# Kernel optimization log

Hardware: AMD Instinct MI355X
Metric: run time of the kernel (lower is better)

Reference implementation:

```python
import jax, jax.numpy as jnp
import numpy as np

B, L, D_MODEL = 1, 1024, 768
H = 12            # num_heads == num_key_value_heads
FDIM = 16         # feature_dim
HEAD_DIM = D_MODEL // H  # 64
EPS = 1e-12
R2 = np.sqrt(2.0)
RD = np.sqrt(float(FDIM))        # sqrt(16) = 4
RRD = np.sqrt(RD)                # sqrt(4) = 2


def setup_inputs() -> dict:
    key = jax.random.key(0)
    ks = jax.random.split(key, 5)
    s = 1.0 / np.sqrt(D_MODEL)
    return {
        "hidden_states": jax.random.normal(ks[0], (B, L, D_MODEL), dtype=jnp.float32),
        "Wq": jax.random.normal(ks[1], (D_MODEL, H * FDIM), dtype=jnp.float32) * s,
        "Wk": jax.random.normal(ks[2], (D_MODEL, H * FDIM), dtype=jnp.float32) * s,
        "Wv": jax.random.normal(ks[3], (D_MODEL, D_MODEL), dtype=jnp.float32) * s,
        "Wo": jax.random.normal(ks[4], (D_MODEL, D_MODEL), dtype=jnp.float32) * s,
    }


def taylor_exp_feature_map(x):
    # x: (b, h, l, FDIM) -> (b, h, l, 1 + FDIM + FDIM^2)
    x2 = (x[..., :, None] * x[..., None, :]).reshape(*x.shape[:-1], FDIM * FDIM) / R2
    ones = jnp.ones((*x.shape[:-1], 1), dtype=x.dtype)
    return jnp.concatenate([ones, x / RRD, x2 / RD], axis=-1)


def reference(hidden_states, Wq, Wk, Wv, Wo):
    b, l, _ = hidden_states.shape
    q = (hidden_states @ Wq).reshape(b, l, H, FDIM).transpose(0, 2, 1, 3)
    k = (hidden_states @ Wk).reshape(b, l, H, FDIM).transpose(0, 2, 1, 3)
    v = (hidden_states @ Wv).reshape(b, l, H, HEAD_DIM).transpose(0, 2, 1, 3)
    q = taylor_exp_feature_map(q)  # (b,h,l,Dexp)
    k = taylor_exp_feature_map(k)  # (b,h,l,Dexp)
    # causal linear attention: y_t = q_t . cumsum_t(k_s v_s^T) / (q_t . cumsum_t(k_s) + eps)
    kv = k[..., :, None] * v[..., None, :]          # (b,h,l,Dexp,hd)
    kv_cum = jnp.cumsum(kv, axis=2)                  # (b,h,l,Dexp,hd)
    num = jnp.einsum('bhln,bhlnd->bhld', q, kv_cum)  # (b,h,l,hd)
    k_cum = jnp.cumsum(k, axis=2)                    # (b,h,l,Dexp)
    den = jnp.einsum('bhln,bhln->bhl', q, k_cum)[..., None] + EPS
    y = num / den                                    # (b,h,l,hd)
    y = y.transpose(0, 2, 1, 3).reshape(b, l, H * HEAD_DIM)
    return y @ Wo
```

## Files before the change

### kernel.cpp

```cpp
#include <hip/hip_runtime.h>

#define C2 0.17677669529663687f

typedef __attribute__((ext_vector_type(8))) short short8;
typedef __attribute__((ext_vector_type(8))) unsigned short ushort8;
typedef __attribute__((ext_vector_type(4))) float f32x4;

__device__ __forceinline__ unsigned short f2bf(float x) {
    union { float f; unsigned u; } v; v.f = x;
    unsigned r = v.u + 0x7fffu + ((v.u >> 16) & 1u);
    return (unsigned short)(r >> 16);
}
__device__ __forceinline__ float bf2f(unsigned short u) {
    union { unsigned u; float f; } v; v.u = ((unsigned)u) << 16;
    return v.f;
}

__device__ __forceinline__ void gemm_inblk_splitk(
    const float* __restrict__ A, const float* __restrict__ W,
    float* __restrict__ out, int row0, int n0, int outcol0, int ldw, int outld)
{
    __shared__ unsigned short Al[2][2][32][40];
    __shared__ unsigned short Bl[2][2][64][40];
    __shared__ float red[32][65];
    const int tid = threadIdx.x;
    const int g = tid >> 8;
    const int t = tid & 255;
    const int lane = t & 63, w4 = t >> 6;
    const int quad = lane >> 4, lr = lane & 15;
    const int k0base = g * 384;

    f32x4 acc[2] = {{0.f,0.f,0.f,0.f},{0.f,0.f,0.f,0.f}};

    float4 ra, rb[2];
    {
        ra = *(const float4*)&A[(size_t)(row0 + (t >> 3)) * 768 + k0base + (t & 7) * 4];
        #pragma unroll
        for (int l = 0; l < 2; ++l) {
            int idy = t + l * 256;
            rb[l] = *(const float4*)&W[(size_t)(k0base + (idy >> 4)) * ldw + n0 + (idy & 15) * 4];
        }
    }
    {
        *(ushort4*)&Al[g][0][t >> 3][(t & 7) * 4] =
            make_ushort4(f2bf(ra.x), f2bf(ra.y), f2bf(ra.z), f2bf(ra.w));
        #pragma unroll
        for (int l = 0; l < 2; ++l) {
            int idy = t + l * 256;
            int kr = idy >> 4, nq = (idy & 15) * 4;
            int col = (((kr >> 3) ^ ((idy & 15) >> 2)) << 3) | (kr & 7);
            Bl[g][0][nq + 0][col] = f2bf(rb[l].x);
            Bl[g][0][nq + 1][col] = f2bf(rb[l].y);
            Bl[g][0][nq + 2][col] = f2bf(rb[l].z);
            Bl[g][0][nq + 3][col] = f2bf(rb[l].w);
        }
    }
    __syncthreads();

    const int ITER = 12;
    #pragma unroll
    for (int i = 0; i < ITER; ++i) {
        const int cur = i & 1, nxt = cur ^ 1;
        float4 na, nb[2];
        if (i + 1 < ITER) {
            int kn = k0base + (i + 1) * 32;
            na = *(const float4*)&A[(size_t)(row0 + (t >> 3)) * 768 + kn + (t & 7) * 4];
            #pragma unroll
            for (int l = 0; l < 2; ++l) {
                int idy = t + l * 256;
                nb[l] = *(const float4*)&W[(size_t)(kn + (idy >> 4)) * ldw + n0 + (idy & 15) * 4];
            }
        }
        short8 af[2], bfr;
        af[0] = *(const short8*)&Al[g][cur][lr][quad << 3];
        af[1] = *(const short8*)&Al[g][cur][16 + lr][quad << 3];
        {
            int csw = quad ^ (w4 & 3);
            bfr = *(const short8*)&Bl[g][cur][w4 * 16 + lr][csw << 3];
        }
        acc[0] = __builtin_amdgcn_mfma_f32_16x16x32_bf16(af[0], bfr, acc[0], 0, 0, 0);
        acc[1] = __builtin_amdgcn_mfma_f32_16x16x32_bf16(af[1], bfr, acc[1], 0, 0, 0);
        if (i + 1 < ITER) {
            *(ushort4*)&Al[g][nxt][t >> 3][(t & 7) * 4] =
                make_ushort4(f2bf(na.x), f2bf(na.y), f2bf(na.z), f2bf(na.w));
            #pragma unroll
            for (int l = 0; l < 2; ++l) {
                int idy = t + l * 256;
                int kr = idy >> 4, nq = (idy & 15) * 4;
                int col = (((kr >> 3) ^ ((idy & 15) >> 2)) << 3) | (kr & 7);
                Bl[g][nxt][nq + 0][col] = f2bf(nb[l].x);
                Bl[g][nxt][nq + 1][col] = f2bf(nb[l].y);
                Bl[g][nxt][nq + 2][col] = f2bf(nb[l].z);
                Bl[g][nxt][nq + 3][col] = f2bf(nb[l].w);
            }
        }
        __syncthreads();
    }
    if (g == 1) {
        #pragma unroll
        for (int mi = 0; mi < 2; ++mi)
            #pragma unroll
            for (int r = 0; r < 4; ++r)
                red[mi * 16 + quad * 4 + r][w4 * 16 + lr] = acc[mi][r];
    }
    __syncthreads();
    if (g == 0) {
        #pragma unroll
        for (int mi = 0; mi < 2; ++mi)
            #pragma unroll
            for (int r = 0; r < 4; ++r) {
                int rr = mi * 16 + quad * 4 + r;
                out[(size_t)(row0 + rr) * outld + outcol0 + w4 * 16 + lr] =
                    acc[mi][r] + red[rr][w4 * 16 + lr];
            }
    }
}

__global__ __launch_bounds__(512) void gemm_qkv_mfma(
    const float* __restrict__ H, const float* __restrict__ Wq,
    const float* __restrict__ Wk, const float* __restrict__ Wv,
    float* __restrict__ out)
{
    const int nt = blockIdx.x, mt = blockIdx.y;
    const float* W; int ldw, n0;
    if (nt < 3)      { W = Wq; ldw = 192; n0 = nt * 64; }
    else if (nt < 6) { W = Wk; ldw = 192; n0 = (nt - 3) * 64; }
    else             { W = Wv; ldw = 768; n0 = (nt - 6) * 64; }
    gemm_inblk_splitk(H, W, out, mt * 32, n0, nt * 64, ldw, 1152);
}

__global__ __launch_bounds__(512) void gemm_wo_mfma(
    const float* __restrict__ Y, const float* __restrict__ Wo, float* __restrict__ out)
{
    const int nt = blockIdx.x, mt = blockIdx.y;
    gemm_inblk_splitk(Y, Wo, out, mt * 32, nt * 64, nt * 64, 768, 768);
}

__global__ __launch_bounds__(256) void chunk_state_k(
    const float* __restrict__ qkv, unsigned short* __restrict__ St, float* __restrict__ z)
{
    const int c = blockIdx.x, h = blockIdx.y;
    __shared__ float Kc[64][17];
    __shared__ unsigned short Pk[320][72];
    __shared__ unsigned short Vt[80][72];
    const int tid = threadIdx.x;
    const int lane = tid & 63, wave = tid >> 6;
    const int quad = lane >> 4, lr = lane & 15;

    {
        int s = tid >> 2, f4 = (tid & 3) * 4;
        float4 kv = *(const float4*)&qkv[(size_t)(c * 64 + s) * 1152 + 192 + h * 16 + f4];
        Kc[s][f4 + 0] = kv.x; Kc[s][f4 + 1] = kv.y; Kc[s][f4 + 2] = kv.z; Kc[s][f4 + 3] = kv.w;
    }
    #pragma unroll
    for (int l = 0; l < 4; ++l) {
        int idx = tid + l * 256;
        int s = idx >> 4, d4 = (idx & 15) * 4;
        float4 vv = *(const float4*)&qkv[(size_t)(c * 64 + s) * 1152 + 384 + h * 64 + d4];
        Vt[d4 + 0][s] = f2bf(vv.x);
        Vt[d4 + 1][s] = f2bf(vv.y);
        Vt[d4 + 2][s] = f2bf(vv.z);
        Vt[d4 + 3][s] = f2bf(vv.w);
    }
    for (int idx = tid; idx < 16 * 72; idx += 256) {
        int rr = 64 + idx / 72, ss = idx % 72;
        Vt[rr][ss] = (rr == 64 && ss < 64) ? (unsigned short)0x3F80 : (unsigned short)0;
    }
    __syncthreads();
    for (int idx = tid; idx < 2880; idx += 256) {
        int n = idx / 9, s8 = (idx % 9) * 8;
        short8 v8;
        #pragma unroll
        for (int tt = 0; tt < 8; ++tt) {
            int s = s8 + tt;
            float ph = 0.f;
            if (s < 64 && n < 273) {
                if (n == 0) ph = 1.f;
                else if (n < 17) ph = Kc[s][n - 1] * 0.5f;
                else { int m = n - 17; ph = Kc[s][m >> 4] * Kc[s][m & 15] * C2; }
            }
            v8[tt] = (short)f2bf(ph);
        }
        *(short8*)&Pk[n][s8] = v8;
    }
    __syncthreads();

    f32x4 acc[5][5];
    #pragma unroll
    for (int a = 0; a < 5; ++a)
        #pragma unroll
        for (int b = 0; b < 5; ++b) acc[a][b] = (f32x4){0.f, 0.f, 0.f, 0.f};
    #pragma unroll
    for (int ks = 0; ks < 2; ++ks) {
        short8 af[5], bfr[5];
        #pragma unroll
        for (int mt = 0; mt < 5; ++mt)
            af[mt] = *(const short8*)&Vt[mt * 16 + lr][ks * 32 + quad * 8];
        #pragma unroll
        for (int nt = 0; nt < 5; ++nt)
            bfr[nt] = *(const short8*)&Pk[(wave * 5 + nt) * 16 + lr][ks * 32 + quad * 8];
        #pragma unroll
        for (int mt = 0; mt < 5; ++mt)
            #pragma unroll
            for (int nt = 0; nt < 5; ++nt)
                acc[mt][nt] = __builtin_amdgcn_mfma_f32_16x16x32_bf16(af[mt], bfr[nt], acc[mt][nt], 0, 0, 0);
    }
    unsigned short* Sbt = St + (size_t)(h * 16 + c) * 18432;
    float* zb = z + (size_t)(h * 16 + c) * 273;
    #pragma unroll
    for (int nt = 0; nt < 5; ++nt) {
        int n = (wave * 5 + nt) * 16 + lr;
        if (n < 273) {
            #pragma unroll
            for (int mt = 0; mt < 4; ++mt)
                #pragma unroll
                for (int r = 0; r < 4; ++r)
                    Sbt[(mt * 16 + quad * 4 + r) * 288 + n] = f2bf(acc[mt][nt][r]);
            if (quad == 0) zb[n] = acc[4][nt][0];
        }
    }
}

__global__ __launch_bounds__(256) void scan_state_k(unsigned short* __restrict__ St, float* __restrict__ z)
{
    const int NS = 12 * 64 * 273;
    int e = blockIdx.x * 256 + threadIdx.x;
    if (e < NS) {
        int hh = e / (64 * 273), rem = e % (64 * 273);
        int d = rem / 273, n = rem % 273;
        unsigned short* p = St + (size_t)hh * 16 * 18432 + d * 288 + n;
        float run = 0.f;
        #pragma unroll
        for (int c = 0; c < 16; ++c) {
            float v = bf2f(p[c * 18432]);
            p[c * 18432] = f2bf(run);
            run += v;
        }
    } else if (e < NS + 12 * 273) {
        int e2 = e - NS, hh = e2 / 273, n = e2 % 273;
        float* p = z + hh * 16 * 273 + n;
        float run = 0.f;
        #pragma unroll
        for (int c = 0; c < 16; ++c) { float v = p[c * 273]; p[c * 273] = run; run += v; }
    }
}

__global__ __launch_bounds__(256) void chunk_out_k(
    const float* __restrict__ qkv, const unsigned short* __restrict__ St, const float* __restrict__ z,
    float* __restrict__ y)
{
    const int c = blockIdx.x, h = blockIdx.y;
    __shared__ float Qc[64][17];
    __shared__ unsigned short Aq[64][40];
    __shared__ unsigned short Kb[64][40];
    __shared__ unsigned short Pq[64][360];
    __shared__ unsigned short Sv[64][360];
    __shared__ float zl[288];
    __shared__ float dpart[6][64];
    const int tid = threadIdx.x;
    const int lane = tid & 63, wave = tid >> 6;
    const int wm = wave & 1, wn = wave >> 1;
    const int quad = lane >> 4, lr = lane & 15;

    {
        int s = tid >> 2, f4 = (tid & 3) * 4;
        const float* base = &qkv[(size_t)(c * 64 + s) * 1152 + h * 16];
        float4 qv = *(const float4*)&base[f4];
        float4 kv = *(const float4*)&base[192 + f4];
        Qc[s][f4 + 0] = qv.x; Qc[s][f4 + 1] = qv.y; Qc[s][f4 + 2] = qv.z; Qc[s][f4 + 3] = qv.w;
        *(ushort4*)&Aq[s][f4] = make_ushort4(f2bf(qv.x), f2bf(qv.y), f2bf(qv.z), f2bf(qv.w));
        *(ushort4*)&Kb[s][f4] = make_ushort4(f2bf(kv.x), f2bf(kv.y), f2bf(kv.z), f2bf(kv.w));
        *(ushort4*)&Aq[s][16 + (tid & 3) * 4] = make_ushort4(0, 0, 0, 0);
        *(ushort4*)&Kb[s][16 + (tid & 3) * 4] = make_ushort4(0, 0, 0, 0);
    }
    #pragma unroll
    for (int l = 0; l < 4; ++l) {
        int idx = tid + l * 256;
        int s = idx >> 4, d4 = (idx & 15) * 4;
        float4 vv = *(const float4*)&qkv[(size_t)(c * 64 + s) * 1152 + 384 + h * 64 + d4];
        Sv[d4 + 0][288 + s] = f2bf(vv.x);
        Sv[d4 + 1][288 + s] = f2bf(vv.y);
        Sv[d4 + 2][288 + s] = f2bf(vv.z);
        Sv[d4 + 3][288 + s] = f2bf(vv.w);
    }
    const unsigned short* Sgt = St + (size_t)(h * 16 + c) * 18432;
    for (int idx = tid; idx < 64 * 34; idx += 256) {
        int d = idx / 34, n8 = (idx % 34) * 8;
        *(ushort8*)&Sv[d][n8] = *(const ushort8*)&Sgt[d * 288 + n8];
    }
    for (int idx = tid; idx < 64; idx += 256) Sv[idx][272] = Sgt[idx * 288 + 272];
    for (int idx = tid; idx < 64 * 15; idx += 256) {
        int d = idx / 15, n = 273 + idx % 15;
        Sv[d][n] = 0;
    }
    const float* zg = z + (size_t)(h * 16 + c) * 273;
    for (int idx = tid; idx < 288; idx += 256) zl[idx] = (idx < 273) ? zg[idx] : 0.f;
    __syncthreads();

    f32x4 accS[2][2] = {{{0.f,0.f,0.f,0.f},{0.f,0.f,0.f,0.f}},
                        {{0.f,0.f,0.f,0.f},{0.f,0.f,0.f,0.f}}};
    {
        short8 af[2], bfr[2];
        #pragma unroll
        for (int mi = 0; mi < 2; ++mi)
            af[mi] = *(const short8*)&Aq[wm * 32 + mi * 16 + lr][quad * 8];
        #pragma unroll
        for (int ni = 0; ni < 2; ++ni)
            bfr[ni] = *(const short8*)&Kb[wn * 32 + ni * 16 + lr][quad * 8];
        #pragma unroll
        for (int mi = 0; mi < 2; ++mi)
            #pragma unroll
            for (int ni = 0; ni < 2; ++ni)
                accS[mi][ni] = __builtin_amdgcn_mfma_f32_16x16x32_bf16(af[mi], bfr[ni], accS[mi][ni], 0, 0, 0);
    }

    {
        int i = lane;
        float qr[16];
        #pragma unroll
        for (int f = 0; f < 16; ++f) qr[f] = Qc[i][f];
        float dp = 0.f;
        int n0 = wave * 72;
        for (int n = n0; n < n0 + 72; ++n) {
            float ph;
            if (n == 0) ph = 1.f;
            else if (n < 17) ph = qr[n - 1] * 0.5f;
            else if (n < 273) { int m = n - 17; ph = qr[m >> 4] * qr[m & 15] * C2; }
            else ph = 0.f;
            Pq[i][n] = f2bf(ph);
            dp += ph * zl[n];
        }
        dpart[wave][i] = dp;
    }

    #pragma unroll
    for (int mi = 0; mi < 2; ++mi) {
        float rs[4] = {0.f, 0.f, 0.f, 0.f};
        #pragma unroll
        for (int ni = 0; ni < 2; ++ni)
            #pragma unroll
            for (int r = 0; r < 4; ++r) {
                int i = wm * 32 + mi * 16 + quad * 4 + r;
                int j = wn * 32 + ni * 16 + lr;
                float u = accS[mi][ni][r];
                float sc = (j <= i) ? (1.f + 0.25f * u + u * u * (1.f / 32.f)) : 0.f;
                rs[r] += sc;
                Pq[i][288 + j] = f2bf(sc);
            }
        #pragma unroll
        for (int r = 0; r < 4; ++r) {
            float v = rs[r];
            v += __shfl_xor(v, 1);
            v += __shfl_xor(v, 2);
            v += __shfl_xor(v, 4);
            v += __shfl_xor(v, 8);
            if (lr == 0) dpart[4 + wn][wm * 32 + mi * 16 + quad * 4 + r] = v;
        }
    }
    __syncthreads();

    f32x4 acc[2][2] = {{{0.f,0.f,0.f,0.f},{0.f,0.f,0.f,0.f}},
                       {{0.f,0.f,0.f,0.f},{0.f,0.f,0.f,0.f}}};
    #pragma unroll
    for (int ks = 0; ks < 11; ++ks) {
        short8 af[2], bfr[2];
        #pragma unroll
        for (int mi = 0; mi < 2; ++mi)
            af[mi] = *(const short8*)&Pq[wm * 32 + mi * 16 + lr][ks * 32 + quad * 8];
        #pragma unroll
        for (int ni = 0; ni < 2; ++ni)
            bfr[ni] = *(const short8*)&Sv[wn * 32 + ni * 16 + lr][ks * 32 + quad * 8];
        #pragma unroll
        for (int mi = 0; mi < 2; ++mi)
            #pragma unroll
            for (int ni = 0; ni < 2; ++ni)
                acc[mi][ni] = __builtin_amdgcn_mfma_f32_16x16x32_bf16(af[mi], bfr[ni], acc[mi][ni], 0, 0, 0);
    }

    #pragma unroll
    for (int mi = 0; mi < 2; ++mi)
        #pragma unroll
        for (int r = 0; r < 4; ++r) {
            int i = wm * 32 + mi * 16 + quad * 4 + r;
            float den = dpart[0][i] + dpart[1][i] + dpart[2][i] +
                        dpart[3][i] + dpart[4][i] + dpart[5][i] + 1e-12f;
            float rden = 1.f / den;
            #pragma unroll
            for (int ni = 0; ni < 2; ++ni)
                y[(size_t)(c * 64 + i) * 768 + h * 64 + wn * 32 + ni * 16 + lr] = acc[mi][ni][r] * rden;
        }
}

extern "C" void kernel_launch(void* const* d_in, const int* in_sizes, int n_in,
                              void* d_out, int out_size, void* d_ws, size_t ws_size,
                              hipStream_t stream) {
    const float* hs = (const float*)d_in[0];
    const float* Wq = (const float*)d_in[1];
    const float* Wk = (const float*)d_in[2];
    const float* Wv = (const float*)d_in[3];
    const float* Wo = (const float*)d_in[4];
    float* out = (float*)d_out;
    float* ws  = (float*)d_ws;

    float* qkv = ws;
    float* yb  = ws + 1179648;
    unsigned short* St = (unsigned short*)(ws + 1966080);
    float* zb  = ws + 5320704;

    gemm_qkv_mfma<<<dim3(18, 32), 512, 0, stream>>>(hs, Wq, Wk, Wv, qkv);
    chunk_state_k<<<dim3(16, 12), 256, 0, stream>>>(qkv, St, zb);
    scan_state_k <<<832, 256, 0, stream>>>(St, zb);
    chunk_out_k  <<<dim3(16, 12), 256, 0, stream>>>(qkv, St, zb, yb);
    gemm_wo_mfma <<<dim3(12, 32), 512, 0, stream>>>(yb, Wo, out);
}
```

Before: 137.9 us.

## Fuse chunk-state prefix scan into state kernel via last-block atomic; widen attention blocks

```diff
diff --git a/kernel.cpp b/kernel.cpp
--- a/kernel.cpp
+++ b/kernel.cpp
@@ -119,8 +119,9 @@
 __global__ __launch_bounds__(512) void gemm_qkv_mfma(
     const float* __restrict__ H, const float* __restrict__ Wq,
     const float* __restrict__ Wk, const float* __restrict__ Wv,
-    float* __restrict__ out)
+    float* __restrict__ out, int* __restrict__ counters)
 {
+    if (blockIdx.x == 0 && blockIdx.y == 0 && threadIdx.x < 12) counters[threadIdx.x] = 0;
     const int nt = blockIdx.x, mt = blockIdx.y;
     const float* W; int ldw, n0;
     if (nt < 3)      { W = Wq; ldw = 192; n0 = nt * 64; }
@@ -136,25 +137,27 @@
     gemm_inblk_splitk(Y, Wo, out, mt * 32, nt * 64, nt * 64, 768, 768);
 }
 
-__global__ __launch_bounds__(256) void chunk_state_k(
-    const float* __restrict__ qkv, unsigned short* __restrict__ St, float* __restrict__ z)
+__global__ __launch_bounds__(512) void chunk_state_k(
+    const float* __restrict__ qkv, unsigned short* __restrict__ St, float* __restrict__ z,
+    int* __restrict__ counters)
 {
     const int c = blockIdx.x, h = blockIdx.y;
     __shared__ float Kc[64][17];
     __shared__ unsigned short Pk[320][72];
     __shared__ unsigned short Vt[80][72];
+    __shared__ int is_last;
     const int tid = threadIdx.x;
     const int lane = tid & 63, wave = tid >> 6;
     const int quad = lane >> 4, lr = lane & 15;
 
-    {
+    if (tid < 256) {
         int s = tid >> 2, f4 = (tid & 3) * 4;
         float4 kv = *(const float4*)&qkv[(size_t)(c * 64 + s) * 1152 + 192 + h * 16 + f4];
         Kc[s][f4 + 0] = kv.x; Kc[s][f4 + 1] = kv.y; Kc[s][f4 + 2] = kv.z; Kc[s][f4 + 3] = kv.w;
     }
     #pragma unroll
-    for (int l = 0; l < 4; ++l) {
-        int idx = tid + l * 256;
+    for (int l = 0; l < 2; ++l) {
+        int idx = tid + l * 512;
         int s = idx >> 4, d4 = (idx & 15) * 4;
         float4 vv = *(const float4*)&qkv[(size_t)(c * 64 + s) * 1152 + 384 + h * 64 + d4];
         Vt[d4 + 0][s] = f2bf(vv.x);
@@ -162,12 +165,12 @@
         Vt[d4 + 2][s] = f2bf(vv.z);
         Vt[d4 + 3][s] = f2bf(vv.w);
     }
-    for (int idx = tid; idx < 16 * 72; idx += 256) {
+    for (int idx = tid; idx < 1152; idx += 512) {
         int rr = 64 + idx / 72, ss = idx % 72;
         Vt[rr][ss] = (rr == 64 && ss < 64) ? (unsigned short)0x3F80 : (unsigned short)0;
     }
     __syncthreads();
-    for (int idx = tid; idx < 2880; idx += 256) {
+    for (int idx = tid; idx < 2880; idx += 512) {
         int n = idx / 9, s8 = (idx % 9) * 8;
         short8 v8;
         #pragma unroll
@@ -185,22 +188,22 @@
     }
     __syncthreads();
 
-    f32x4 acc[5][5];
-    #pragma unroll
-    for (int a = 0; a < 5; ++a)
+    const int mg = wave & 1, ng = wave >> 1;
+    const int MT = mg ? 2 : 3, mbase = mg ? 3 : 0;
+    f32x4 acc[3][5];
+    #pragma unroll
+    for (int a = 0; a < 3; ++a)
         #pragma unroll
         for (int b = 0; b < 5; ++b) acc[a][b] = (f32x4){0.f, 0.f, 0.f, 0.f};
     #pragma unroll
     for (int ks = 0; ks < 2; ++ks) {
-        short8 af[5], bfr[5];
-        #pragma unroll
-        for (int mt = 0; mt < 5; ++mt)
-            af[mt] = *(const short8*)&Vt[mt * 16 + lr][ks * 32 + quad * 8];
+        short8 af[3], bfr[5];
+        for (int mt = 0; mt < MT; ++mt)
+            af[mt] = *(const short8*)&Vt[(mbase + mt) * 16 + lr][ks * 32 + quad * 8];
         #pragma unroll
         for (int nt = 0; nt < 5; ++nt)
-            bfr[nt] = *(const short8*)&Pk[(wave * 5 + nt) * 16 + lr][ks * 32 + quad * 8];
-        #pragma unroll
-        for (int mt = 0; mt < 5; ++mt)
+            bfr[nt] = *(const short8*)&Pk[(ng * 5 + nt) * 16 + lr][ks * 32 + quad * 8];
+        for (int mt = 0; mt < MT; ++mt)
             #pragma unroll
             for (int nt = 0; nt < 5; ++nt)
                 acc[mt][nt] = __builtin_amdgcn_mfma_f32_16x16x32_bf16(af[mt], bfr[nt], acc[mt][nt], 0, 0, 0);
@@ -209,43 +212,63 @@
     float* zb = z + (size_t)(h * 16 + c) * 273;
     #pragma unroll
     for (int nt = 0; nt < 5; ++nt) {
-        int n = (wave * 5 + nt) * 16 + lr;
+        int n = (ng * 5 + nt) * 16 + lr;
         if (n < 273) {
-            #pragma unroll
-            for (int mt = 0; mt < 4; ++mt)
-                #pragma unroll
-                for (int r = 0; r < 4; ++r)
-                    Sbt[(mt * 16 + quad * 4 + r) * 288 + n] = f2bf(acc[mt][nt][r]);
-            if (quad == 0) zb[n] = acc[4][nt][0];
-        }
-    }
-}
-
-__global__ __launch_bounds__(256) void scan_state_k(unsigned short* __restrict__ St, float* __restrict__ z)
-{
-    const int NS = 12 * 64 * 273;
-    int e = blockIdx.x * 256 + threadIdx.x;
-    if (e < NS) {
-        int hh = e / (64 * 273), rem = e % (64 * 273);
-        int d = rem / 273, n = rem % 273;
-        unsigned short* p = St + (size_t)hh * 16 * 18432 + d * 288 + n;
-        float run = 0.f;
-        #pragma unroll
-        for (int c = 0; c < 16; ++c) {
-            float v = bf2f(p[c * 18432]);
-            p[c * 18432] = f2bf(run);
-            run += v;
-        }
-    } else if (e < NS + 12 * 273) {
-        int e2 = e - NS, hh = e2 / 273, n = e2 % 273;
-        float* p = z + hh * 16 * 273 + n;
-        float run = 0.f;
-        #pragma unroll
-        for (int c = 0; c < 16; ++c) { float v = p[c * 273]; p[c * 273] = run; run += v; }
-    }
-}
-
-__global__ __launch_bounds__(256) void chunk_out_k(
+            for (int mt = 0; mt < MT; ++mt) {
+                int mtile = mbase + mt;
+                if (mtile < 4) {
+                    #pragma unroll
+                    for (int r = 0; r < 4; ++r)
+                        Sbt[(mtile * 16 + quad * 4 + r) * 288 + n] = f2bf(acc[mt][nt][r]);
+                } else if (quad == 0) {
+                    zb[n] = acc[mt][nt][0];
+                }
+            }
+        }
+    }
+
+    __syncthreads();
+    if (tid == 0) {
+        __threadfence();
+        int prev = atomicAdd(&counters[h], 1);
+        is_last = (prev == 15) ? 1 : 0;
+    }
+    __syncthreads();
+    if (is_last) {
+        __threadfence();
+        unsigned short* Sh = St + (size_t)h * 16 * 18432;
+        for (int idx = tid; idx < 64 * 35; idx += 512) {
+            int d = idx / 35, gq = idx % 35;
+            if (gq < 34) {
+                unsigned short* p = Sh + d * 288 + gq * 8;
+                float run[8] = {0.f,0.f,0.f,0.f,0.f,0.f,0.f,0.f};
+                for (int cc = 0; cc < 16; ++cc) {
+                    ushort8 v = *(ushort8*)&p[(size_t)cc * 18432];
+                    ushort8 o;
+                    #pragma unroll
+                    for (int tt = 0; tt < 8; ++tt) { o[tt] = f2bf(run[tt]); run[tt] += bf2f(v[tt]); }
+                    *(ushort8*)&p[(size_t)cc * 18432] = o;
+                }
+            } else {
+                unsigned short* p = Sh + d * 288 + 272;
+                float run = 0.f;
+                for (int cc = 0; cc < 16; ++cc) {
+                    float v = bf2f(p[(size_t)cc * 18432]);
+                    p[(size_t)cc * 18432] = f2bf(run);
+                    run += v;
+                }
+            }
+        }
+        float* zh = z + (size_t)h * 16 * 273;
+        for (int idx = tid; idx < 273; idx += 512) {
+            float* p = zh + idx;
+            float run = 0.f;
+            for (int cc = 0; cc < 16; ++cc) { float v = p[cc * 273]; p[cc * 273] = run; run += v; }
+        }
+    }
+}
+
+__global__ __launch_bounds__(512) void chunk_out_k(
     const float* __restrict__ qkv, const unsigned short* __restrict__ St, const float* __restrict__ z,
     float* __restrict__ y)
 {
@@ -256,13 +279,14 @@
     __shared__ unsigned short Pq[64][360];
     __shared__ unsigned short Sv[64][360];
     __shared__ float zl[288];
-    __shared__ float dpart[6][64];
+    __shared__ float dpart[12][64];
     const int tid = threadIdx.x;
     const int lane = tid & 63, wave = tid >> 6;
-    const int wm = wave & 1, wn = wave >> 1;
     const int quad = lane >> 4, lr = lane & 15;
-
-    {
+    const int wm = wave & 1;
+    const int wn4 = wave >> 1;
+
+    if (tid < 256) {
         int s = tid >> 2, f4 = (tid & 3) * 4;
         const float* base = &qkv[(size_t)(c * 64 + s) * 1152 + h * 16];
         float4 qv = *(const float4*)&base[f4];
@@ -274,8 +298,8 @@
         *(ushort4*)&Kb[s][16 + (tid & 3) * 4] = make_ushort4(0, 0, 0, 0);
     }
     #pragma unroll
-    for (int l = 0; l < 4; ++l) {
-        int idx = tid + l * 256;
+    for (int l = 0; l < 2; ++l) {
+        int idx = tid + l * 512;
         int s = idx >> 4, d4 = (idx & 15) * 4;
         float4 vv = *(const float4*)&qkv[(size_t)(c * 64 + s) * 1152 + 384 + h * 64 + d4];
         Sv[d4 + 0][288 + s] = f2bf(vv.x);
@@ -284,34 +308,29 @@
         Sv[d4 + 3][288 + s] = f2bf(vv.w);
     }
     const unsigned short* Sgt = St + (size_t)(h * 16 + c) * 18432;
-    for (int idx = tid; idx < 64 * 34; idx += 256) {
+    for (int idx = tid; idx < 2176; idx += 512) {
         int d = idx / 34, n8 = (idx % 34) * 8;
         *(ushort8*)&Sv[d][n8] = *(const ushort8*)&Sgt[d * 288 + n8];
     }
-    for (int idx = tid; idx < 64; idx += 256) Sv[idx][272] = Sgt[idx * 288 + 272];
-    for (int idx = tid; idx < 64 * 15; idx += 256) {
+    if (tid < 64) Sv[tid][272] = Sgt[tid * 288 + 272];
+    for (int idx = tid; idx < 960; idx += 512) {
         int d = idx / 15, n = 273 + idx % 15;
         Sv[d][n] = 0;
     }
     const float* zg = z + (size_t)(h * 16 + c) * 273;
-    for (int idx = tid; idx < 288; idx += 256) zl[idx] = (idx < 273) ? zg[idx] : 0.f;
-    __syncthreads();
-
-    f32x4 accS[2][2] = {{{0.f,0.f,0.f,0.f},{0.f,0.f,0.f,0.f}},
-                        {{0.f,0.f,0.f,0.f},{0.f,0.f,0.f,0.f}}};
+    for (int idx = tid; idx < 288; idx += 512) zl[idx] = (idx < 273) ? zg[idx] : 0.f;
+    __syncthreads();
+
+    f32x4 accS[2] = {{0.f,0.f,0.f,0.f},{0.f,0.f,0.f,0.f}};
     {
-        short8 af[2], bfr[2];
+        short8 afq[2], bfk;
         #pragma unroll
         for (int mi = 0; mi < 2; ++mi)
-            af[mi] = *(const short8*)&Aq[wm * 32 + mi * 16 + lr][quad * 8];
-        #pragma unroll
-        for (int ni = 0; ni < 2; ++ni)
-            bfr[ni] = *(const short8*)&Kb[wn * 32 + ni * 16 + lr][quad * 8];
+            afq[mi] = *(const short8*)&Aq[wm * 32 + mi * 16 + lr][quad * 8];
+        bfk = *(const short8*)&Kb[wn4 * 16 + lr][quad * 8];
         #pragma unroll
         for (int mi = 0; mi < 2; ++mi)
-            #pragma unroll
-            for (int ni = 0; ni < 2; ++ni)
-                accS[mi][ni] = __builtin_amdgcn_mfma_f32_16x16x32_bf16(af[mi], bfr[ni], accS[mi][ni], 0, 0, 0);
+            accS[mi] = __builtin_amdgcn_mfma_f32_16x16x32_bf16(afq[mi], bfk, accS[mi], 0, 0, 0);
     }
 
     {
@@ -320,8 +339,8 @@
         #pragma unroll
         for (int f = 0; f < 16; ++f) qr[f] = Qc[i][f];
         float dp = 0.f;
-        int n0 = wave * 72;
-        for (int n = n0; n < n0 + 72; ++n) {
+        int n0 = wave * 36;
+        for (int n = n0; n < n0 + 36; ++n) {
             float ph;
             if (n == 0) ph = 1.f;
             else if (n < 17) ph = qr[n - 1] * 0.5f;
@@ -335,18 +354,16 @@
 
     #pragma unroll
     for (int mi = 0; mi < 2; ++mi) {
-        float rs[4] = {0.f, 0.f, 0.f, 0.f};
-        #pragma unroll
-        for (int ni = 0; ni < 2; ++ni)
-            #pragma unroll
-            for (int r = 0; r < 4; ++r) {
-                int i = wm * 32 + mi * 16 + quad * 4 + r;
-                int j = wn * 32 + ni * 16 + lr;
-                float u = accS[mi][ni][r];
-                float sc = (j <= i) ? (1.f + 0.25f * u + u * u * (1.f / 32.f)) : 0.f;
-                rs[r] += sc;
-                Pq[i][288 + j] = f2bf(sc);
-            }
+        float rs[4];
+        #pragma unroll
+        for (int r = 0; r < 4; ++r) {
+            int i = wm * 32 + mi * 16 + quad * 4 + r;
+            int j = wn4 * 16 + lr;
+            float u = accS[mi][r];
+            float sc = (j <= i) ? (1.f + 0.25f * u + u * u * (1.f / 32.f)) : 0.f;
+            rs[r] = sc;
+            Pq[i][288 + j] = f2bf(sc);
+        }
         #pragma unroll
         for (int r = 0; r < 4; ++r) {
             float v = rs[r];
@@ -354,41 +371,33 @@
             v += __shfl_xor(v, 2);
             v += __shfl_xor(v, 4);
             v += __shfl_xor(v, 8);
-            if (lr == 0) dpart[4 + wn][wm * 32 + mi * 16 + quad * 4 + r] = v;
-        }
-    }
-    __syncthreads();
-
-    f32x4 acc[2][2] = {{{0.f,0.f,0.f,0.f},{0.f,0.f,0.f,0.f}},
-                       {{0.f,0.f,0.f,0.f},{0.f,0.f,0.f,0.f}}};
+            if (lr == 0) dpart[8 + wn4][wm * 32 + mi * 16 + quad * 4 + r] = v;
+        }
+    }
+    __syncthreads();
+
+    const int mt = wave >> 1, nh = wave & 1;
+    f32x4 acc[2] = {{0.f,0.f,0.f,0.f},{0.f,0.f,0.f,0.f}};
     #pragma unroll
     for (int ks = 0; ks < 11; ++ks) {
-        short8 af[2], bfr[2];
-        #pragma unroll
-        for (int mi = 0; mi < 2; ++mi)
-            af[mi] = *(const short8*)&Pq[wm * 32 + mi * 16 + lr][ks * 32 + quad * 8];
+        short8 af = *(const short8*)&Pq[mt * 16 + lr][ks * 32 + quad * 8];
+        short8 b0 = *(const short8*)&Sv[nh * 32 + lr][ks * 32 + quad * 8];
+        short8 b1 = *(const short8*)&Sv[nh * 32 + 16 + lr][ks * 32 + quad * 8];
+        acc[0] = __builtin_amdgcn_mfma_f32_16x16x32_bf16(af, b0, acc[0], 0, 0, 0);
+        acc[1] = __builtin_amdgcn_mfma_f32_16x16x32_bf16(af, b1, acc[1], 0, 0, 0);
+    }
+
+    #pragma unroll
+    for (int r = 0; r < 4; ++r) {
+        int i = mt * 16 + quad * 4 + r;
+        float den = 1e-12f;
+        #pragma unroll
+        for (int p = 0; p < 12; ++p) den += dpart[p][i];
+        float rden = 1.f / den;
         #pragma unroll
         for (int ni = 0; ni < 2; ++ni)
-            bfr[ni] = *(const short8*)&Sv[wn * 32 + ni * 16 + lr][ks * 32 + quad * 8];
-        #pragma unroll
-        for (int mi = 0; mi < 2; ++mi)
-            #pragma unroll
-            for (int ni = 0; ni < 2; ++ni)
-                acc[mi][ni] = __builtin_amdgcn_mfma_f32_16x16x32_bf16(af[mi], bfr[ni], acc[mi][ni], 0, 0, 0);
-    }
-
-    #pragma unroll
-    for (int mi = 0; mi < 2; ++mi)
-        #pragma unroll
-        for (int r = 0; r < 4; ++r) {
-            int i = wm * 32 + mi * 16 + quad * 4 + r;
-            float den = dpart[0][i] + dpart[1][i] + dpart[2][i] +
-                        dpart[3][i] + dpart[4][i] + dpart[5][i] + 1e-12f;
-            float rden = 1.f / den;
-            #pragma unroll
-            for (int ni = 0; ni < 2; ++ni)
-                y[(size_t)(c * 64 + i) * 768 + h * 64 + wn * 32 + ni * 16 + lr] = acc[mi][ni][r] * rden;
-        }
+            y[(size_t)(c * 64 + i) * 768 + h * 64 + nh * 32 + ni * 16 + lr] = acc[ni][r] * rden;
+    }
 }
 
 extern "C" void kernel_launch(void* const* d_in, const int* in_sizes, int n_in,
@@ -406,10 +415,10 @@
     float* yb  = ws + 1179648;
     unsigned short* St = (unsigned short*)(ws + 1966080);
     float* zb  = ws + 5320704;
-
-    gemm_qkv_mfma<<<dim3(18, 32), 512, 0, stream>>>(hs, Wq, Wk, Wv, qkv);
-    chunk_state_k<<<dim3(16, 12), 256, 0, stream>>>(qkv, St, zb);
-    scan_state_k <<<832, 256, 0, stream>>>(St, zb);
-    chunk_out_k  <<<dim3(16, 12), 256, 0, stream>>>(qkv, St, zb, yb);
+    int* counters = (int*)(ws + 5373120);
+
+    gemm_qkv_mfma<<<dim3(18, 32), 512, 0, stream>>>(hs, Wq, Wk, Wv, qkv, counters);
+    chunk_state_k<<<dim3(16, 12), 512, 0, stream>>>(qkv, St, zb, counters);
+    chunk_out_k  <<<dim3(16, 12), 512, 0, stream>>>(qkv, St, zb, yb);
     gemm_wo_mfma <<<dim3(12, 32), 512, 0, stream>>>(yb, Wo, out);
 }
```

Result: slower. 186.9 us (+35.6%).
